# Performance work log

Hardware: AMD Instinct MI355X
Metric: run time of the kernel (lower is better)

The kernel has to match this reference:

```python
import jax, jax.numpy as jnp
import numpy as np

B, T, D, H, L, F, V = 2, 512, 512, 8, 6, 2048, 32000
EPS = 1e-6


def _ln(x, g, b):
    m = x.mean(-1, keepdims=True)
    v = ((x - m) ** 2).mean(-1, keepdims=True)
    return (x - m) / jnp.sqrt(v + EPS) * g + b


def _mha(qx, kx, qkv_w, qkv_b, ow, ob, mask):
    # Wide heads: each head has dim D (Linear(D, H*D) projections, Linear(H*D, D) output).
    Bq, Tq, _ = qx.shape
    def proj(xx, w, bi):
        return (xx @ w + bi).reshape(Bq, Tq, H, D).transpose(0, 2, 1, 3)  # (B,H,T,D)
    q = proj(qx, qkv_w[0], qkv_b[0])
    k = proj(kx, qkv_w[1], qkv_b[1])
    v = proj(kx, qkv_w[2], qkv_b[2])
    s = jnp.einsum('bhqd,bhkd->bhqk', q, k) / jnp.sqrt(jnp.float32(D))
    if mask is not None:
        s = jnp.where(mask, s, -jnp.inf)
    w = jax.nn.softmax(s, axis=-1)
    o = jnp.einsum('bhqk,bhkd->bhqd', w, v).transpose(0, 2, 1, 3).reshape(Bq, Tq, H * D)
    return o @ ow + ob


def _pe(t, d):
    pos = jnp.arange(t, dtype=jnp.float32)[:, None]
    wl = jnp.exp(jnp.arange(0, d, 2, dtype=jnp.float32) / d * -jnp.log(10000.0))
    pe = jnp.zeros((t, d), dtype=jnp.float32)
    pe = pe.at[:, 0::2].set(jnp.sin(pos * wl))
    pe = pe.at[:, 1::2].set(jnp.cos(pos * wl))
    return pe


def _forward(x, y, enc_emb, dec_emb, enc_qkv_w, enc_qkv_b, enc_out_w, enc_out_b,
             enc_ln1_g, enc_ln1_b, enc_ff_w1, enc_ff_b1, enc_ff_w2, enc_ff_b2,
             enc_ln2_g, enc_ln2_b, dec_sa_qkv_w, dec_sa_qkv_b, dec_sa_out_w, dec_sa_out_b,
             dec_ln1_g, dec_ln1_b, dec_ca_qkv_w, dec_ca_qkv_b, dec_ca_out_w, dec_ca_out_b,
             dec_ln2_g, dec_ln2_b, dec_ff_w1, dec_ff_b1, dec_ff_w2, dec_ff_b2,
             dec_ln3_g, dec_ln3_b, head_w, head_b):
    pe = _pe(T, D)
    scale = jnp.sqrt(jnp.float32(D))
    # ---- encoder ----
    h = enc_emb[x] * scale + pe  # (B,T,D)
    for i in range(L):
        a = _mha(h, h, enc_qkv_w[i], enc_qkv_b[i], enc_out_w[i], enc_out_b[i], None)
        h = _ln(a + h, enc_ln1_g[i], enc_ln1_b[i])
        f = jax.nn.relu(h @ enc_ff_w1[i] + enc_ff_b1[i]) @ enc_ff_w2[i] + enc_ff_b2[i]
        h = _ln(f + h, enc_ln2_g[i], enc_ln2_b[i])
    # ---- decoder ----
    causal = jnp.tril(jnp.ones((T, T), dtype=bool))[None, None]  # (1,1,T,T)
    d = dec_emb[y] * scale + pe
    for i in range(L):
        a = _mha(d, d, dec_sa_qkv_w[i], dec_sa_qkv_b[i], dec_sa_out_w[i], dec_sa_out_b[i], causal)
        d = _ln(a + d, dec_ln1_g[i], dec_ln1_b[i])
        c = _mha(d, h, dec_ca_qkv_w[i], dec_ca_qkv_b[i], dec_ca_out_w[i], dec_ca_out_b[i], None)
        d = _ln(c + d, dec_ln2_g[i], dec_ln2_b[i])
        f = jax.nn.relu(d @ dec_ff_w1[i] + dec_ff_b1[i]) @ dec_ff_w2[i] + dec_ff_b2[i]
        d = _ln(f + d, dec_ln3_g[i], dec_ln3_b[i])
    return d @ head_w + head_b  # (B,T,V) logits


def setup_inputs() -> dict:
    key = jax.random.key(0)
    ks = iter(jax.random.split(key, 40))
    def nrm(shape):
        return jax.random.normal(next(ks), shape, dtype=jnp.float32) * 0.02
    HD = H * D
    return {
        'x': jax.random.randint(next(ks), (B, T), 0, V, dtype=jnp.int32),
        'y': jax.random.randint(next(ks), (B, T), 0, V, dtype=jnp.int32),
        'enc_emb': nrm((V, D)), 'dec_emb': nrm((V, D)),
        'enc_qkv_w': nrm((L, 3, D, HD)), 'enc_qkv_b': jnp.zeros((L, 3, HD)),
        'enc_out_w': nrm((L, HD, D)), 'enc_out_b': jnp.zeros((L, D)),
        'enc_ln1_g': jnp.ones((L, D)), 'enc_ln1_b': jnp.zeros((L, D)),
        'enc_ff_w1': nrm((L, D, F)), 'enc_ff_b1': jnp.zeros((L, F)),
        'enc_ff_w2': nrm((L, F, D)), 'enc_ff_b2': jnp.zeros((L, D)),
        'enc_ln2_g': jnp.ones((L, D)), 'enc_ln2_b': jnp.zeros((L, D)),
        'dec_sa_qkv_w': nrm((L, 3, D, HD)), 'dec_sa_qkv_b': jnp.zeros((L, 3, HD)),
        'dec_sa_out_w': nrm((L, HD, D)), 'dec_sa_out_b': jnp.zeros((L, D)),
        'dec_ln1_g': jnp.ones((L, D)), 'dec_ln1_b': jnp.zeros((L, D)),
        'dec_ca_qkv_w': nrm((L, 3, D, HD)), 'dec_ca_qkv_b': jnp.zeros((L, 3, HD)),
        'dec_ca_out_w': nrm((L, HD, D)), 'dec_ca_out_b': jnp.zeros((L, D)),
        'dec_ln2_g': jnp.ones((L, D)), 'dec_ln2_b': jnp.zeros((L, D)),
        'dec_ff_w1': nrm((L, D, F)), 'dec_ff_b1': jnp.zeros((L, F)),
        'dec_ff_w2': nrm((L, F, D)), 'dec_ff_b2': jnp.zeros((L, D)),
        'dec_ln3_g': jnp.ones((L, D)), 'dec_ln3_b': jnp.zeros((L, D)),
        'head_w': nrm((D, V)), 'head_b': jnp.zeros((V,)),
    }


def reference(x, y, enc_emb, dec_emb, enc_qkv_w, enc_qkv_b, enc_out_w, enc_out_b,
              enc_ln1_g, enc_ln1_b, enc_ff_w1, enc_ff_b1, enc_ff_w2, enc_ff_b2,
              enc_ln2_g, enc_ln2_b, dec_sa_qkv_w, dec_sa_qkv_b, dec_sa_out_w, dec_sa_out_b,
              dec_ln1_g, dec_ln1_b, dec_ca_qkv_w, dec_ca_qkv_b, dec_ca_out_w, dec_ca_out_b,
              dec_ln2_g, dec_ln2_b, dec_ff_w1, dec_ff_b1, dec_ff_w2, dec_ff_b2,
              dec_ln3_g, dec_ln3_b, head_w, head_b):
    return _forward(x, y, enc_emb, dec_emb, enc_qkv_w, enc_qkv_b, enc_out_w, enc_out_b,
                    enc_ln1_g, enc_ln1_b, enc_ff_w1, enc_ff_b1, enc_ff_w2, enc_ff_b2,
                    enc_ln2_g, enc_ln2_b, dec_sa_qkv_w, dec_sa_qkv_b, dec_sa_out_w, dec_sa_out_b,
                    dec_ln1_g, dec_ln1_b, dec_ca_qkv_w, dec_ca_qkv_b, dec_ca_out_w, dec_ca_out_b,
                    dec_ln2_g, dec_ln2_b, dec_ff_w1, dec_ff_b1, dec_ff_w2, dec_ff_b2,
                    dec_ln3_g, dec_ln3_b, head_w, head_b)
```

## Files before the change

kernel.cpp:

```cpp
#include <hip/hip_runtime.h>
#include <hip/hip_bf16.h>

#define B_ 2
#define T_ 512
#define D_ 512
#define H_ 8
#define L_ 6
#define F_ 2048
#define V_ 32000
#define BT_ (B_ * T_)
#define HD_ (H_ * D_)
#define BH_ (B_ * H_)

typedef __attribute__((ext_vector_type(8))) short short8;
typedef __attribute__((ext_vector_type(4))) short short4v;
typedef __attribute__((ext_vector_type(4))) float f32x4;

__device__ __forceinline__ short f2b(float f) {
  __hip_bfloat16 h = __float2bfloat16(f);
  short u; __builtin_memcpy(&u, &h, 2); return u;
}
__device__ __forceinline__ void store_c(float* p, float v) { *p = v; }
__device__ __forceinline__ void store_c(short* p, float v) { *p = f2b(v); }

__global__ __launch_bounds__(256) void embed_kernel(
    const int* __restrict__ tok, const float* __restrict__ emb,
    float* __restrict__ out, short* __restrict__ out16)
{
  const int row = blockIdx.x;
  const int t = row & (T_ - 1);
  const int token = tok[row];
  const float* e = emb + (size_t)token * D_;
  float* o = out + (size_t)row * D_;
  short* o16 = out16 + (size_t)row * D_;
  const float scale = sqrtf((float)D_);
  const float nl = -logf(10000.0f);
  for (int d = threadIdx.x; d < D_; d += 256) {
    int i = d >> 1;
    float wl = expf(nl * (2.0f * (float)i) / (float)D_);
    float ang = (float)t * wl;
    float pe = (d & 1) ? cosf(ang) : sinf(ang);
    float v = e[d] * scale + pe;
    o[d] = v; o16[d] = f2b(v);
  }
}

template<bool BTM, typename OutT, int BM>
__global__ __launch_bounds__(256, 3) void mfma_gemm(
    const short* __restrict__ A, long lda, long a_hi, long a_lo,
    const void* __restrict__ Bv, long ldb, long b_hi, long b_lo,
    OutT* __restrict__ C, long ldc, long c_hi, long c_lo, long pstride,
    short* __restrict__ Ct, int trans_hh,
    int K, int nh, int ksplit, float scale,
    const float* __restrict__ bias, long bias_stride)
{
  constexpr int SA = BM + 1;
  constexpr int AU = BM / 32;
  constexpr int WRN = (BM == 128) ? 2 : 1;
  constexpr int WN  = 128 / (4 / WRN);
  constexpr int NR  = WN / 16;
  __shared__ short8 As8[8 * SA];
  __shared__ short8 Bs8[8 * 129];
  const int tid = threadIdx.x;
  const int bh = blockIdx.z / ksplit;
  const int kz = blockIdx.z - bh * ksplit;
  const int bb = bh / nh, hh = bh - bb * nh;
  const short* Ab = A + (long)bb * a_hi + (long)hh * a_lo;
  const short* Bbs = (const short*)Bv + (long)bb * b_hi + (long)hh * b_lo;
  const float* Bbf = (const float*)Bv + (long)bb * b_hi + (long)hh * b_lo;
  OutT* Cb = C + (long)bb * c_hi + (long)hh * c_lo + (long)kz * pstride;

  const int gx = gridDim.x, gy = gridDim.y;
  const int nwg = gx * gy;
  int lin = blockIdx.y * gx + blockIdx.x;
  {
    const int xcd = lin & 7, idx = lin >> 3;
    const int q = nwg >> 3, r = nwg & 7;
    lin = (xcd < r ? xcd * (q + 1) : r * (q + 1) + (xcd - r) * q) + idx;
  }
  const int bn = (lin / gy) * 128;
  const int bm = (lin % gy) * BM;

  const int klen = K / ksplit, kbase = kz * klen;
  const int lane = tid & 63, wid = tid >> 6;
  const int wr = (WRN == 2) ? (wid >> 1) : 0;
  const int wc = (WRN == 2) ? (wid & 1) : wid;
  const int lg = lane >> 4, r16 = lane & 15;

  int arow[AU], acol[AU];
#pragma unroll
  for (int u = 0; u < AU; ++u) { int o = u * 256 + tid; arow[u] = o >> 3; acol[u] = o & 7; }
  const int ncol = tid & 127, nsh = tid >> 7;

  short8 pa[AU];
  short8 pbt[4];
  float  pbn[4][8];

  auto load = [&](int k0) {
#pragma unroll
    for (int u = 0; u < AU; ++u)
      pa[u] = *(const short8*)(Ab + (long)(bm + arow[u]) * lda + (k0 + acol[u] * 8));
    if constexpr (BTM) {
#pragma unroll
      for (int u = 0; u < 4; ++u)
        pbt[u] = *(const short8*)(Bbs + (long)(bn + (u * 256 + tid) / 8) * ldb + (k0 + ((u * 256 + tid) & 7) * 8));
    } else {
      const float* s = Bbf + (long)(k0 + nsh * 32) * ldb + (bn + ncol);
#pragma unroll
      for (int i = 0; i < 4; ++i)
#pragma unroll
        for (int j = 0; j < 8; ++j)
          pbn[i][j] = s[(long)(i * 8 + j) * ldb];
    }
  };
  auto stage = [&]() {
#pragma unroll
    for (int u = 0; u < AU; ++u) As8[acol[u] * SA + arow[u]] = pa[u];
    if constexpr (BTM) {
#pragma unroll
      for (int u = 0; u < 4; ++u)
        Bs8[((u * 256 + tid) & 7) * 129 + (u * 256 + tid) / 8] = pbt[u];
    } else {
#pragma unroll
      for (int i = 0; i < 4; ++i) {
        short8 v;
#pragma unroll
        for (int j = 0; j < 8; ++j) v[j] = f2b(pbn[i][j]);
        Bs8[(nsh * 4 + i) * 129 + ncol] = v;
      }
    }
  };

  f32x4 acc[4][NR] = {};
  auto domfma = [&]() {
#pragma unroll
    for (int kb = 0; kb < 2; ++kb) {
      const int cha = (kb * 4 + lg) * SA;
      const int chb = (kb * 4 + lg) * 129;
      short8 a0 = As8[cha + wr * 64 +  0 + r16];
      short8 a1 = As8[cha + wr * 64 + 16 + r16];
      short8 a2 = As8[cha + wr * 64 + 32 + r16];
      short8 a3 = As8[cha + wr * 64 + 48 + r16];
#pragma unroll
      for (int n = 0; n < NR; ++n) {
        short8 bfr = Bs8[chb + wc * WN + n * 16 + r16];
        acc[0][n] = __builtin_amdgcn_mfma_f32_16x16x32_bf16(a0, bfr, acc[0][n], 0, 0, 0);
        acc[1][n] = __builtin_amdgcn_mfma_f32_16x16x32_bf16(a1, bfr, acc[1][n], 0, 0, 0);
        acc[2][n] = __builtin_amdgcn_mfma_f32_16x16x32_bf16(a2, bfr, acc[2][n], 0, 0, 0);
        acc[3][n] = __builtin_amdgcn_mfma_f32_16x16x32_bf16(a3, bfr, acc[3][n], 0, 0, 0);
      }
    }
  };

  load(kbase);
  stage();
  __syncthreads();
  const int nsteps = klen >> 6;
  for (int t = 0; t < nsteps; ++t) {
    const bool more = (t + 1 < nsteps);
    if (more) load(kbase + (t + 1) * 64);
    domfma();
    if (more) { __syncthreads(); stage(); __syncthreads(); }
  }

  const float* bp = bias ? bias + (long)hh * bias_stride : nullptr;
  if (hh == trans_hh) {
#pragma unroll
    for (int m = 0; m < 4; ++m)
#pragma unroll
      for (int n = 0; n < NR; ++n) {
        const int col = bn + wc * WN + n * 16 + r16;
        const float badd = bp ? bp[col] : 0.0f;
        short4v sv;
#pragma unroll
        for (int rr = 0; rr < 4; ++rr) sv[rr] = f2b(acc[m][n][rr] * scale + badd);
        *(short4v*)(Ct + (long)col * BT_ + (bm + wr * 64 + m * 16 + lg * 4)) = sv;
      }
  } else {
#pragma unroll
    for (int m = 0; m < 4; ++m)
#pragma unroll
      for (int rr = 0; rr < 4; ++rr) {
        const int row = bm + wr * 64 + m * 16 + lg * 4 + rr;
        OutT* crow = Cb + (long)row * ldc + bn + wc * WN + r16;
#pragma unroll
        for (int n = 0; n < NR; ++n) {
          float v = acc[m][n][rr] * scale;
          if (bp) v += bp[bn + wc * WN + n * 16 + r16];
          store_c(&crow[n * 16], v);
        }
      }
  }
}

__global__ __launch_bounds__(256) void reduce_bias_relu_bf16(
    const float* __restrict__ P, long pstride, int ks,
    const float* __restrict__ bias, short* __restrict__ out, long mn, int N)
{
  const long i = ((long)blockIdx.x * 256 + threadIdx.x) * 4;
  if (i >= mn) return;
  float4 s = *(const float4*)(P + i);
  for (int z = 1; z < ks; ++z) {
    float4 t = *(const float4*)(P + (long)z * pstride + i);
    s.x += t.x; s.y += t.y; s.z += t.z; s.w += t.w;
  }
  const int col = (int)(i % N);
  s.x += bias[col]; s.y += bias[col + 1]; s.z += bias[col + 2]; s.w += bias[col + 3];
  short4v o;
  o[0] = f2b(fmaxf(s.x, 0.f)); o[1] = f2b(fmaxf(s.y, 0.f));
  o[2] = f2b(fmaxf(s.z, 0.f)); o[3] = f2b(fmaxf(s.w, 0.f));
  *(short4v*)(out + i) = o;
}

__global__ __launch_bounds__(256) void reduce_ln_kernel(
    const float* __restrict__ P, long pstride, int ks,
    const float* __restrict__ bias, float* __restrict__ hbuf, short* __restrict__ h16,
    const float* __restrict__ gam, const float* __restrict__ bet)
{
  __shared__ float red[256];
  const int row = blockIdx.x, tid = threadIdx.x;
  const long base = (long)row * D_;
  float s0 = hbuf[base + tid] + bias[tid];
  float s1 = hbuf[base + tid + 256] + bias[tid + 256];
  for (int z = 0; z < ks; ++z) {
    s0 += P[(long)z * pstride + base + tid];
    s1 += P[(long)z * pstride + base + tid + 256];
  }
  red[tid] = s0 + s1; __syncthreads();
  for (int o = 128; o > 0; o >>= 1) { if (tid < o) red[tid] += red[tid + o]; __syncthreads(); }
  const float mean = red[0] * (1.0f / D_); __syncthreads();
  const float d0 = s0 - mean, d1 = s1 - mean;
  red[tid] = d0 * d0 + d1 * d1; __syncthreads();
  for (int o = 128; o > 0; o >>= 1) { if (tid < o) red[tid] += red[tid + o]; __syncthreads(); }
  const float inv = rsqrtf(red[0] * (1.0f / D_) + 1e-6f);
  const float v0 = d0 * inv * gam[tid] + bet[tid];
  const float v1 = d1 * inv * gam[tid + 256] + bet[tid + 256];
  hbuf[base + tid] = v0;       h16[base + tid] = f2b(v0);
  hbuf[base + tid + 256] = v1; h16[base + tid + 256] = f2b(v1);
}

__global__ __launch_bounds__(256) void softmax_kernel(
    const float* __restrict__ S, short* __restrict__ P, int causal)
{
  __shared__ float red[256];
  const int q = blockIdx.x, bh = blockIdx.y, tid = threadIdx.x;
  const float* row = S + ((size_t)bh * T_ + q) * T_;
  short* prow = P + ((size_t)bh * T_ + q) * T_;
  const int n = causal ? (q + 1) : T_;
  const float v0 = row[tid], v1 = row[tid + 256];
  const bool in0 = tid < n, in1 = (tid + 256) < n;
  red[tid] = fmaxf(in0 ? v0 : -3.0e38f, in1 ? v1 : -3.0e38f);
  __syncthreads();
  for (int o = 128; o > 0; o >>= 1) { if (tid < o) red[tid] = fmaxf(red[tid], red[tid + o]); __syncthreads(); }
  const float m = red[0]; __syncthreads();
  const float e0 = in0 ? expf(v0 - m) : 0.0f;
  const float e1 = in1 ? expf(v1 - m) : 0.0f;
  red[tid] = e0 + e1; __syncthreads();
  for (int o = 128; o > 0; o >>= 1) { if (tid < o) red[tid] += red[tid + o]; __syncthreads(); }
  const float inv = 1.0f / red[0];
  prow[tid] = f2b(e0 * inv);
  prow[tid + 256] = f2b(e1 * inv);
}

extern "C" void kernel_launch(void* const* d_in, const int* in_sizes, int n_in,
                              void* d_out, int out_size, void* d_ws, size_t ws_size,
                              hipStream_t stream)
{
  const int*   x         = (const int*)d_in[0];
  const int*   y         = (const int*)d_in[1];
  const float* enc_emb   = (const float*)d_in[2];
  const float* dec_emb   = (const float*)d_in[3];
  const float* enc_qkv_w = (const float*)d_in[4];
  const float* enc_qkv_b = (const float*)d_in[5];
  const float* enc_out_w = (const float*)d_in[6];
  const float* enc_out_b = (const float*)d_in[7];
  const float* enc_ln1_g = (const float*)d_in[8];
  const float* enc_ln1_b = (const float*)d_in[9];
  const float* enc_ff_w1 = (const float*)d_in[10];
  const float* enc_ff_b1 = (const float*)d_in[11];
  const float* enc_ff_w2 = (const float*)d_in[12];
  const float* enc_ff_b2 = (const float*)d_in[13];
  const float* enc_ln2_g = (const float*)d_in[14];
  const float* enc_ln2_b = (const float*)d_in[15];
  const float* dec_sa_qkv_w = (const float*)d_in[16];
  const float* dec_sa_qkv_b = (const float*)d_in[17];
  const float* dec_sa_out_w = (const float*)d_in[18];
  const float* dec_sa_out_b = (const float*)d_in[19];
  const float* dec_ln1_g = (const float*)d_in[20];
  const float* dec_ln1_b = (const float*)d_in[21];
  const float* dec_ca_qkv_w = (const float*)d_in[22];
  const float* dec_ca_qkv_b = (const float*)d_in[23];
  const float* dec_ca_out_w = (const float*)d_in[24];
  const float* dec_ca_out_b = (const float*)d_in[25];
  const float* dec_ln2_g = (const float*)d_in[26];
  const float* dec_ln2_b = (const float*)d_in[27];
  const float* dec_ff_w1 = (const float*)d_in[28];
  const float* dec_ff_b1 = (const float*)d_in[29];
  const float* dec_ff_w2 = (const float*)d_in[30];
  const float* dec_ff_b2 = (const float*)d_in[31];
  const float* dec_ln3_g = (const float*)d_in[32];
  const float* dec_ln3_b = (const float*)d_in[33];
  const float* head_w    = (const float*)d_in[34];
  const float* head_b    = (const float*)d_in[35];
  float* out = (float*)d_out;

  char* wsb = (char*)d_ws;
  size_t off = 0;
  auto carve = [&](size_t bytes) { char* p = wsb + off; off += (bytes + 255) & ~255ull; return p; };
  float* h    = (float*)carve((size_t)BT_ * D_ * 4);
  float* dd   = (float*)carve((size_t)BT_ * D_ * 4);
  short* hb16 = (short*)carve((size_t)BT_ * D_ * 2);
  short* db16 = (short*)carve((size_t)BT_ * D_ * 2);
  short* Qb   = (short*)carve((size_t)BT_ * HD_ * 2);
  short* Kb   = (short*)carve((size_t)BT_ * HD_ * 2);
  short* Vt   = (short*)carve((size_t)HD_ * BT_ * 2);
  float* Sb   = (float*)carve((size_t)BH_ * T_ * T_ * 4);
  short* Pb   = (short*)carve((size_t)BH_ * T_ * T_ * 2);
  short* Ob   = Qb;
  short* mid  = Qb;
  (void)ws_size;

  dim3 blk(256);
  const long TT  = (long)T_ * T_;
  const long THD = (long)T_ * HD_;
  const long WQKV = (long)D_ * HD_;

  auto gemm = [&](bool bt, bool of32, bool bm64,
                  const short* A, long lda, long a_hi, long a_lo,
                  const void* Bp, long ldb, long b_hi, long b_lo,
                  void* Cp, long ldc, long c_hi, long c_lo, long pstride,
                  short* Ct, int trans_hh,
                  int M, int N, int K, int batch, int nh, int ksplit,
                  float scale, const float* bias, long bstride) {
    dim3 grd(N / 128, M / (bm64 ? 64 : 128), batch * ksplit);
    if (bm64) {
      if (bt) {
        if (of32) mfma_gemm<true , float, 64><<<grd, blk, 0, stream>>>(A, lda, a_hi, a_lo, Bp, ldb, b_hi, b_lo,
            (float*)Cp, ldc, c_hi, c_lo, pstride, Ct, trans_hh, K, nh, ksplit, scale, bias, bstride);
        else      mfma_gemm<true , short, 64><<<grd, blk, 0, stream>>>(A, lda, a_hi, a_lo, Bp, ldb, b_hi, b_lo,
            (short*)Cp, ldc, c_hi, c_lo, pstride, Ct, trans_hh, K, nh, ksplit, scale, bias, bstride);
      } else {
        if (of32) mfma_gemm<false, float, 64><<<grd, blk, 0, stream>>>(A, lda, a_hi, a_lo, Bp, ldb, b_hi, b_lo,
            (float*)Cp, ldc, c_hi, c_lo, pstride, Ct, trans_hh, K, nh, ksplit, scale, bias, bstride);
        else      mfma_gemm<false, short, 64><<<grd, blk, 0, stream>>>(A, lda, a_hi, a_lo, Bp, ldb, b_hi, b_lo,
            (short*)Cp, ldc, c_hi, c_lo, pstride, Ct, trans_hh, K, nh, ksplit, scale, bias, bstride);
      }
    } else {
      if (of32) mfma_gemm<false, float, 128><<<grd, blk, 0, stream>>>(A, lda, a_hi, a_lo, Bp, ldb, b_hi, b_lo,
          (float*)Cp, ldc, c_hi, c_lo, pstride, Ct, trans_hh, K, nh, ksplit, scale, bias, bstride);
      else      mfma_gemm<false, short, 128><<<grd, blk, 0, stream>>>(A, lda, a_hi, a_lo, Bp, ldb, b_hi, b_lo,
          (short*)Cp, ldc, c_hi, c_lo, pstride, Ct, trans_hh, K, nh, ksplit, scale, bias, bstride);
    }
  };

  auto attention = [&](const short* qsrc, const short* kvsrc, bool self,
                       const float* qkvw, const float* qkvb,
                       const float* ow, const float* ob,
                       float* resid, short* resid16, int causal,
                       const float* lng, const float* lnb) {
    if (self) {
      gemm(false, false, true, qsrc, D_, 0, 0, qkvw, HD_, 0, WQKV,
           Qb, HD_, 0, (long)(Kb - Qb), 0, Vt, 2,
           BT_, HD_, D_, 3, 3, 1, 1.0f, qkvb, HD_);
    } else {
      gemm(false, false, true, qsrc, D_, 0, 0, qkvw, HD_, 0, 0,
           Qb, HD_, 0, 0, 0, nullptr, -1,
           BT_, HD_, D_, 1, 1, 1, 1.0f, qkvb, 0);
      gemm(false, false, true, kvsrc, D_, 0, 0, qkvw + WQKV, HD_, 0, WQKV,
           Kb, HD_, 0, 0, 0, Vt, 1,
           BT_, HD_, D_, 2, 2, 1, 1.0f, qkvb + HD_, HD_);
    }
    gemm(true, true, true, Qb, HD_, THD, D_, Kb, HD_, THD, D_,
         Sb, T_, (long)H_ * TT, TT, 0, nullptr, -1,
         T_, T_, D_, BH_, H_, 1, 0.044194173824159216f, nullptr, 0);
    softmax_kernel<<<dim3(T_, BH_), blk, 0, stream>>>(Sb, Pb, causal);
    gemm(true, false, true, Pb, T_, (long)H_ * TT, TT, Vt, BT_, T_, (long)D_ * BT_,
         Ob, HD_, THD, D_, 0, nullptr, -1,
         T_, D_, T_, BH_, H_, 1, 1.0f, nullptr, 0);
    gemm(false, true, true, Ob, HD_, 0, 0, ow, D_, 0, 0,
         Sb, D_, 0, 0, (long)BT_ * D_, nullptr, -1,
         BT_, D_, HD_, 1, 1, 8, 1.0f, nullptr, 0);
    reduce_ln_kernel<<<dim3(BT_), blk, 0, stream>>>(
        Sb, (long)BT_ * D_, 8, ob, resid, resid16, lng, lnb);
  };

  auto ffn = [&](float* resid, short* resid16,
                 const float* w1, const float* b1,
                 const float* w2, const float* b2,
                 const float* lng, const float* lnb) {
    gemm(false, true, true, resid16, D_, 0, 0, w1, F_, 0, 0,
         Sb, F_, 0, 0, (long)BT_ * F_, nullptr, -1,
         BT_, F_, D_, 1, 1, 2, 1.0f, nullptr, 0);
    reduce_bias_relu_bf16<<<dim3(BT_ * F_ / 1024), blk, 0, stream>>>(
        Sb, (long)BT_ * F_, 2, b1, mid, (long)BT_ * F_, F_);
    gemm(false, true, true, mid, F_, 0, 0, w2, D_, 0, 0,
         Sb, D_, 0, 0, (long)BT_ * D_, nullptr, -1,
         BT_, D_, F_, 1, 1, 8, 1.0f, nullptr, 0);
    reduce_ln_kernel<<<dim3(BT_), blk, 0, stream>>>(
        Sb, (long)BT_ * D_, 8, b2, resid, resid16, lng, lnb);
  };

  embed_kernel<<<dim3(BT_), blk, 0, stream>>>(x, enc_emb, h, hb16);
  for (int i = 0; i < L_; ++i) {
    attention(hb16, hb16, true,
              enc_qkv_w + (size_t)i * 3 * WQKV, enc_qkv_b + (size_t)i * 3 * HD_,
              enc_out_w + (size_t)i * HD_ * D_, enc_out_b + (size_t)i * D_,
              h, hb16, 0, enc_ln1_g + (size_t)i * D_, enc_ln1_b + (size_t)i * D_);
    ffn(h, hb16, enc_ff_w1 + (size_t)i * D_ * F_, enc_ff_b1 + (size_t)i * F_,
        enc_ff_w2 + (size_t)i * F_ * D_, enc_ff_b2 + (size_t)i * D_,
        enc_ln2_g + (size_t)i * D_, enc_ln2_b + (size_t)i * D_);
  }

  embed_kernel<<<dim3(BT_), blk, 0, stream>>>(y, dec_emb, dd, db16);
  for (int i = 0; i < L_; ++i) {
    attention(db16, db16, true,
              dec_sa_qkv_w + (size_t)i * 3 * WQKV, dec_sa_qkv_b + (size_t)i * 3 * HD_,
              dec_sa_out_w + (size_t)i * HD_ * D_, dec_sa_out_b + (size_t)i * D_,
              dd, db16, 1, dec_ln1_g + (size_t)i * D_, dec_ln1_b + (size_t)i * D_);
    attention(db16, hb16, false,
              dec_ca_qkv_w + (size_t)i * 3 * WQKV, dec_ca_qkv_b + (size_t)i * 3 * HD_,
              dec_ca_out_w + (size_t)i * HD_ * D_, dec_ca_out_b + (size_t)i * D_,
              dd, db16, 0, dec_ln2_g + (size_t)i * D_, dec_ln2_b + (size_t)i * D_);
    ffn(dd, db16, dec_ff_w1 + (size_t)i * D_ * F_, dec_ff_b1 + (size_t)i * F_,
        dec_ff_w2 + (size_t)i * F_ * D_, dec_ff_b2 + (size_t)i * D_,
        dec_ln3_g + (size_t)i * D_, dec_ln3_b + (size_t)i * D_);
  }

  gemm(false, true, false, db16, D_, 0, 0, head_w, V_, 0, 0,
       out, V_, 0, 0, 0, nullptr, -1,
       BT_, V_, D_, 1, 1, 1, 1.0f, head_b, 0);
}
```

Baseline: 2.392 ms.

## Double-buffer GEMM LDS tiles, fuse FFN bias+ReLU, switch most GEMMs to 128-row tiles

The GEMM kernel now keeps two LDS buffers and two register prefetch sets, so global loads for the next two K-steps overlap the MFMA work and one barrier is saved per step. FFN1 drops its split-K fp32 partials and the separate bias/ReLU reduce kernel, writing bf16 output with bias and ReLU applied in the epilogue. Most attention and projection GEMMs move from 64-row to 128-row tiles, which adds transposed-B 128 variants and lowers launch bounds to 2 waves for those tiles. The cost is doubled LDS and more registers, which cuts occupancy and leaves fewer blocks for the smaller GEMMs.

New measurement: 2.465 ms. 3.0% more time.

```diff
diff --git a/kernel.cpp b/kernel.cpp
--- a/kernel.cpp
+++ b/kernel.cpp
@@ -46,21 +46,21 @@
 }
 
 template<bool BTM, typename OutT, int BM>
-__global__ __launch_bounds__(256, 3) void mfma_gemm(
+__global__ __launch_bounds__(256, BM == 128 ? 2 : 3) void mfma_gemm(
     const short* __restrict__ A, long lda, long a_hi, long a_lo,
     const void* __restrict__ Bv, long ldb, long b_hi, long b_lo,
     OutT* __restrict__ C, long ldc, long c_hi, long c_lo, long pstride,
-    short* __restrict__ Ct, int trans_hh,
+    short* __restrict__ Ct, int trans_hh, int relu,
     int K, int nh, int ksplit, float scale,
     const float* __restrict__ bias, long bias_stride)
 {
   constexpr int SA = BM + 1;
   constexpr int AU = BM / 32;
   constexpr int WRN = (BM == 128) ? 2 : 1;
-  constexpr int WN  = 128 / (4 / WRN);
+  constexpr int WN  = (BM == 128) ? 64 : 32;
   constexpr int NR  = WN / 16;
-  __shared__ short8 As8[8 * SA];
-  __shared__ short8 Bs8[8 * 129];
+  __shared__ short8 As8[2 * 8 * SA];
+  __shared__ short8 Bs8[2 * 8 * 129];
   const int tid = threadIdx.x;
   const int bh = blockIdx.z / ksplit;
   const int kz = blockIdx.z - bh * ksplit;
@@ -90,53 +90,60 @@
   int arow[AU], acol[AU];
 #pragma unroll
   for (int u = 0; u < AU; ++u) { int o = u * 256 + tid; arow[u] = o >> 3; acol[u] = o & 7; }
+  int brow[4], bcol[4];
+#pragma unroll
+  for (int u = 0; u < 4; ++u) { int o = u * 256 + tid; brow[u] = o >> 3; bcol[u] = o & 7; }
   const int ncol = tid & 127, nsh = tid >> 7;
 
-  short8 pa[AU];
-  short8 pbt[4];
-  float  pbn[4][8];
-
-  auto load = [&](int k0) {
-#pragma unroll
-    for (int u = 0; u < AU; ++u)
-      pa[u] = *(const short8*)(Ab + (long)(bm + arow[u]) * lda + (k0 + acol[u] * 8));
-    if constexpr (BTM) {
-#pragma unroll
-      for (int u = 0; u < 4; ++u)
-        pbt[u] = *(const short8*)(Bbs + (long)(bn + (u * 256 + tid) / 8) * ldb + (k0 + ((u * 256 + tid) & 7) * 8));
-    } else {
-      const float* s = Bbf + (long)(k0 + nsh * 32) * ldb + (bn + ncol);
-#pragma unroll
-      for (int i = 0; i < 4; ++i)
-#pragma unroll
-        for (int j = 0; j < 8; ++j)
-          pbn[i][j] = s[(long)(i * 8 + j) * ldb];
-    }
-  };
-  auto stage = [&]() {
-#pragma unroll
-    for (int u = 0; u < AU; ++u) As8[acol[u] * SA + arow[u]] = pa[u];
-    if constexpr (BTM) {
-#pragma unroll
-      for (int u = 0; u < 4; ++u)
-        Bs8[((u * 256 + tid) & 7) * 129 + (u * 256 + tid) / 8] = pbt[u];
-    } else {
-#pragma unroll
-      for (int i = 0; i < 4; ++i) {
-        short8 v;
-#pragma unroll
-        for (int j = 0; j < 8; ++j) v[j] = f2b(pbn[i][j]);
-        Bs8[(nsh * 4 + i) * 129 + ncol] = v;
-      }
-    }
-  };
+  short8 pa0[AU], pa1[AU];
+  short8 pbt0[4], pbt1[4];
+  float  pbn0[4][8], pbn1[4][8];
+
+#define LOADSET(PA, PBT, PBN, K0)                                               \
+  {                                                                             \
+    _Pragma("unroll")                                                           \
+    for (int u = 0; u < AU; ++u)                                                \
+      PA[u] = *(const short8*)(Ab + (long)(bm + arow[u]) * lda + ((K0) + acol[u] * 8)); \
+    if constexpr (BTM) {                                                        \
+      _Pragma("unroll")                                                         \
+      for (int u = 0; u < 4; ++u)                                               \
+        PBT[u] = *(const short8*)(Bbs + (long)(bn + brow[u]) * ldb + ((K0) + bcol[u] * 8)); \
+    } else {                                                                    \
+      const float* s_ = Bbf + (long)((K0) + nsh * 32) * ldb + (bn + ncol);      \
+      _Pragma("unroll")                                                         \
+      for (int i = 0; i < 4; ++i)                                               \
+        _Pragma("unroll")                                                       \
+        for (int j = 0; j < 8; ++j)                                             \
+          PBN[i][j] = s_[(long)(i * 8 + j) * ldb];                              \
+    }                                                                           \
+  }
+
+#define STAGESET(PA, PBT, PBN, BUF)                                             \
+  {                                                                             \
+    const int ao_ = (BUF) * 8 * SA, bo_ = (BUF) * 8 * 129;                      \
+    _Pragma("unroll")                                                           \
+    for (int u = 0; u < AU; ++u) As8[ao_ + acol[u] * SA + arow[u]] = PA[u];     \
+    if constexpr (BTM) {                                                        \
+      _Pragma("unroll")                                                         \
+      for (int u = 0; u < 4; ++u) Bs8[bo_ + bcol[u] * 129 + brow[u]] = PBT[u];  \
+    } else {                                                                    \
+      _Pragma("unroll")                                                         \
+      for (int i = 0; i < 4; ++i) {                                             \
+        short8 v_;                                                              \
+        _Pragma("unroll")                                                       \
+        for (int j = 0; j < 8; ++j) v_[j] = f2b(PBN[i][j]);                     \
+        Bs8[bo_ + (nsh * 4 + i) * 129 + ncol] = v_;                             \
+      }                                                                         \
+    }                                                                           \
+  }
 
   f32x4 acc[4][NR] = {};
-  auto domfma = [&]() {
+  auto domfma = [&](int buf) {
+    const int ao = buf * 8 * SA, bo = buf * 8 * 129;
 #pragma unroll
     for (int kb = 0; kb < 2; ++kb) {
-      const int cha = (kb * 4 + lg) * SA;
-      const int chb = (kb * 4 + lg) * 129;
+      const int cha = ao + (kb * 4 + lg) * SA;
+      const int chb = bo + (kb * 4 + lg) * 129;
       short8 a0 = As8[cha + wr * 64 +  0 + r16];
       short8 a1 = As8[cha + wr * 64 + 16 + r16];
       short8 a2 = As8[cha + wr * 64 + 32 + r16];
@@ -152,16 +159,26 @@
     }
   };
 
-  load(kbase);
-  stage();
+  const int nsteps = klen >> 6;
+  LOADSET(pa0, pbt0, pbn0, kbase)
+  STAGESET(pa0, pbt0, pbn0, 0)
+  if (nsteps > 1) LOADSET(pa1, pbt1, pbn1, kbase + 64)
   __syncthreads();
-  const int nsteps = klen >> 6;
-  for (int t = 0; t < nsteps; ++t) {
-    const bool more = (t + 1 < nsteps);
-    if (more) load(kbase + (t + 1) * 64);
-    domfma();
-    if (more) { __syncthreads(); stage(); __syncthreads(); }
-  }
+
+  for (int t = 0; t + 1 < nsteps; t += 2) {
+    if (t + 2 < nsteps) LOADSET(pa0, pbt0, pbn0, kbase + (t + 2) * 64)
+    domfma(0);
+    STAGESET(pa1, pbt1, pbn1, 1)
+    __syncthreads();
+    if (t + 3 < nsteps) LOADSET(pa1, pbt1, pbn1, kbase + (t + 3) * 64)
+    domfma(1);
+    if (t + 2 < nsteps) {
+      STAGESET(pa0, pbt0, pbn0, 0)
+      __syncthreads();
+    }
+  }
+#undef LOADSET
+#undef STAGESET
 
   const float* bp = bias ? bias + (long)hh * bias_stride : nullptr;
   if (hh == trans_hh) {
@@ -187,29 +204,11 @@
         for (int n = 0; n < NR; ++n) {
           float v = acc[m][n][rr] * scale;
           if (bp) v += bp[bn + wc * WN + n * 16 + r16];
+          if (relu) v = fmaxf(v, 0.0f);
           store_c(&crow[n * 16], v);
         }
       }
   }
-}
-
-__global__ __launch_bounds__(256) void reduce_bias_relu_bf16(
-    const float* __restrict__ P, long pstride, int ks,
-    const float* __restrict__ bias, short* __restrict__ out, long mn, int N)
-{
-  const long i = ((long)blockIdx.x * 256 + threadIdx.x) * 4;
-  if (i >= mn) return;
-  float4 s = *(const float4*)(P + i);
-  for (int z = 1; z < ks; ++z) {
-    float4 t = *(const float4*)(P + (long)z * pstride + i);
-    s.x += t.x; s.y += t.y; s.z += t.z; s.w += t.w;
-  }
-  const int col = (int)(i % N);
-  s.x += bias[col]; s.y += bias[col + 1]; s.z += bias[col + 2]; s.w += bias[col + 3];
-  short4v o;
-  o[0] = f2b(fmaxf(s.x, 0.f)); o[1] = f2b(fmaxf(s.y, 0.f));
-  o[2] = f2b(fmaxf(s.z, 0.f)); o[3] = f2b(fmaxf(s.w, 0.f));
-  *(short4v*)(out + i) = o;
 }
 
 __global__ __launch_bounds__(256) void reduce_ln_kernel(
@@ -325,7 +324,7 @@
   const long THD = (long)T_ * HD_;
   const long WQKV = (long)D_ * HD_;
 
-  auto gemm = [&](bool bt, bool of32, bool bm64,
+  auto gemm = [&](bool bt, bool of32, bool bm64, int relu,
                   const short* A, long lda, long a_hi, long a_lo,
                   const void* Bp, long ldb, long b_hi, long b_lo,
                   void* Cp, long ldc, long c_hi, long c_lo, long pstride,
@@ -336,20 +335,27 @@
     if (bm64) {
       if (bt) {
         if (of32) mfma_gemm<true , float, 64><<<grd, blk, 0, stream>>>(A, lda, a_hi, a_lo, Bp, ldb, b_hi, b_lo,
-            (float*)Cp, ldc, c_hi, c_lo, pstride, Ct, trans_hh, K, nh, ksplit, scale, bias, bstride);
+            (float*)Cp, ldc, c_hi, c_lo, pstride, Ct, trans_hh, relu, K, nh, ksplit, scale, bias, bstride);
         else      mfma_gemm<true , short, 64><<<grd, blk, 0, stream>>>(A, lda, a_hi, a_lo, Bp, ldb, b_hi, b_lo,
-            (short*)Cp, ldc, c_hi, c_lo, pstride, Ct, trans_hh, K, nh, ksplit, scale, bias, bstride);
+            (short*)Cp, ldc, c_hi, c_lo, pstride, Ct, trans_hh, relu, K, nh, ksplit, scale, bias, bstride);
       } else {
         if (of32) mfma_gemm<false, float, 64><<<grd, blk, 0, stream>>>(A, lda, a_hi, a_lo, Bp, ldb, b_hi, b_lo,
-            (float*)Cp, ldc, c_hi, c_lo, pstride, Ct, trans_hh, K, nh, ksplit, scale, bias, bstride);
+            (float*)Cp, ldc, c_hi, c_lo, pstride, Ct, trans_hh, relu, K, nh, ksplit, scale, bias, bstride);
         else      mfma_gemm<false, short, 64><<<grd, blk, 0, stream>>>(A, lda, a_hi, a_lo, Bp, ldb, b_hi, b_lo,
-            (short*)Cp, ldc, c_hi, c_lo, pstride, Ct, trans_hh, K, nh, ksplit, scale, bias, bstride);
+            (short*)Cp, ldc, c_hi, c_lo, pstride, Ct, trans_hh, relu, K, nh, ksplit, scale, bias, bstride);
       }
     } else {
-      if (of32) mfma_gemm<false, float, 128><<<grd, blk, 0, stream>>>(A, lda, a_hi, a_lo, Bp, ldb, b_hi, b_lo,
-          (float*)Cp, ldc, c_hi, c_lo, pstride, Ct, trans_hh, K, nh, ksplit, scale, bias, bstride);
-      else      mfma_gemm<false, short, 128><<<grd, blk, 0, stream>>>(A, lda, a_hi, a_lo, Bp, ldb, b_hi, b_lo,
-          (short*)Cp, ldc, c_hi, c_lo, pstride, Ct, trans_hh, K, nh, ksplit, scale, bias, bstride);
+      if (bt) {
+        if (of32) mfma_gemm<true , float, 128><<<grd, blk, 0, stream>>>(A, lda, a_hi, a_lo, Bp, ldb, b_hi, b_lo,
+            (float*)Cp, ldc, c_hi, c_lo, pstride, Ct, trans_hh, relu, K, nh, ksplit, scale, bias, bstride);
+        else      mfma_gemm<true , short, 128><<<grd, blk, 0, stream>>>(A, lda, a_hi, a_lo, Bp, ldb, b_hi, b_lo,
+            (short*)Cp, ldc, c_hi, c_lo, pstride, Ct, trans_hh, relu, K, nh, ksplit, scale, bias, bstride);
+      } else {
+        if (of32) mfma_gemm<false, float, 128><<<grd, blk, 0, stream>>>(A, lda, a_hi, a_lo, Bp, ldb, b_hi, b_lo,
+            (float*)Cp, ldc, c_hi, c_lo, pstride, Ct, trans_hh, relu, K, nh, ksplit, scale, bias, bstride);
+        else      mfma_gemm<false, short, 128><<<grd, blk, 0, stream>>>(A, lda, a_hi, a_lo, Bp, ldb, b_hi, b_lo,
+            (short*)Cp, ldc, c_hi, c_lo, pstride, Ct, trans_hh, relu, K, nh, ksplit, scale, bias, bstride);
+      }
     }
   };
 
@@ -359,25 +365,25 @@
                        float* resid, short* resid16, int causal,
                        const float* lng, const float* lnb) {
     if (self) {
-      gemm(false, false, true, qsrc, D_, 0, 0, qkvw, HD_, 0, WQKV,
+      gemm(false, false, false, 0, qsrc, D_, 0, 0, qkvw, HD_, 0, WQKV,
            Qb, HD_, 0, (long)(Kb - Qb), 0, Vt, 2,
            BT_, HD_, D_, 3, 3, 1, 1.0f, qkvb, HD_);
     } else {
-      gemm(false, false, true, qsrc, D_, 0, 0, qkvw, HD_, 0, 0,
+      gemm(false, false, false, 0, qsrc, D_, 0, 0, qkvw, HD_, 0, 0,
            Qb, HD_, 0, 0, 0, nullptr, -1,
            BT_, HD_, D_, 1, 1, 1, 1.0f, qkvb, 0);
-      gemm(false, false, true, kvsrc, D_, 0, 0, qkvw + WQKV, HD_, 0, WQKV,
+      gemm(false, false, false, 0, kvsrc, D_, 0, 0, qkvw + WQKV, HD_, 0, WQKV,
            Kb, HD_, 0, 0, 0, Vt, 1,
            BT_, HD_, D_, 2, 2, 1, 1.0f, qkvb + HD_, HD_);
     }
-    gemm(true, true, true, Qb, HD_, THD, D_, Kb, HD_, THD, D_,
+    gemm(true, true, false, 0, Qb, HD_, THD, D_, Kb, HD_, THD, D_,
          Sb, T_, (long)H_ * TT, TT, 0, nullptr, -1,
          T_, T_, D_, BH_, H_, 1, 0.044194173824159216f, nullptr, 0);
     softmax_kernel<<<dim3(T_, BH_), blk, 0, stream>>>(Sb, Pb, causal);
-    gemm(true, false, true, Pb, T_, (long)H_ * TT, TT, Vt, BT_, T_, (long)D_ * BT_,
+    gemm(true, false, false, 0, Pb, T_, (long)H_ * TT, TT, Vt, BT_, T_, (long)D_ * BT_,
          Ob, HD_, THD, D_, 0, nullptr, -1,
          T_, D_, T_, BH_, H_, 1, 1.0f, nullptr, 0);
-    gemm(false, true, true, Ob, HD_, 0, 0, ow, D_, 0, 0,
+    gemm(false, true, false, 0, Ob, HD_, 0, 0, ow, D_, 0, 0,
          Sb, D_, 0, 0, (long)BT_ * D_, nullptr, -1,
          BT_, D_, HD_, 1, 1, 8, 1.0f, nullptr, 0);
     reduce_ln_kernel<<<dim3(BT_), blk, 0, stream>>>(
@@ -388,12 +394,10 @@
                  const float* w1, const float* b1,
                  const float* w2, const float* b2,
                  const float* lng, const float* lnb) {
-    gemm(false, true, true, resid16, D_, 0, 0, w1, F_, 0, 0,
-         Sb, F_, 0, 0, (long)BT_ * F_, nullptr, -1,
-         BT_, F_, D_, 1, 1, 2, 1.0f, nullptr, 0);
-    reduce_bias_relu_bf16<<<dim3(BT_ * F_ / 1024), blk, 0, stream>>>(
-        Sb, (long)BT_ * F_, 2, b1, mid, (long)BT_ * F_, F_);
-    gemm(false, true, true, mid, F_, 0, 0, w2, D_, 0, 0,
+    gemm(false, false, true, 1, resid16, D_, 0, 0, w1, F_, 0, 0,
+         mid, F_, 0, 0, 0, nullptr, -1,
+         BT_, F_, D_, 1, 1, 1, 1.0f, b1, 0);
+    gemm(false, true, false, 0, mid, F_, 0, 0, w2, D_, 0, 0,
          Sb, D_, 0, 0, (long)BT_ * D_, nullptr, -1,
          BT_, D_, F_, 1, 1, 8, 1.0f, nullptr, 0);
     reduce_ln_kernel<<<dim3(BT_), blk, 0, stream>>>(
@@ -426,7 +430,7 @@
         dec_ln3_g + (size_t)i * D_, dec_ln3_b + (size_t)i * D_);
   }
 
-  gemm(false, true, false, db16, D_, 0, 0, head_w, V_, 0, 0,
+  gemm(false, true, false, 0, db16, D_, 0, 0, head_w, V_, 0, 0,
        out, V_, 0, 0, 0, nullptr, -1,
        BT_, V_, D_, 1, 1, 1, 1.0f, head_b, 0);
 }
```

## Fuse QK^T with softmax in one kernel and fuse FFN bias+ReLU into GEMM

Applied to the files above, without the earlier changes.

Adds a qksm_kernel that computes Q·K^T scores with MFMA, then applies scaling, causal masking and softmax in registers and writes bf16 probabilities. This replaces the fp32 score GEMM and the separate softmax kernel, and causal blocks skip key tiles that are fully masked. The first FFN GEMM now adds bias and applies ReLU in its epilogue and writes bf16 directly, instead of split-K fp32 partials followed by a reduce kernel. The fused attention kernel holds 32 accumulator tiles per wave and reloads K into LDS for each of 8 chunks, which may raise register pressure and lower occupancy.

Measured after the change: 3.162 ms. +32.2%, slower.

```diff
diff --git a/kernel.cpp b/kernel.cpp
--- a/kernel.cpp
+++ b/kernel.cpp
@@ -50,14 +50,14 @@
     const short* __restrict__ A, long lda, long a_hi, long a_lo,
     const void* __restrict__ Bv, long ldb, long b_hi, long b_lo,
     OutT* __restrict__ C, long ldc, long c_hi, long c_lo, long pstride,
-    short* __restrict__ Ct, int trans_hh,
+    short* __restrict__ Ct, int trans_hh, int relu,
     int K, int nh, int ksplit, float scale,
     const float* __restrict__ bias, long bias_stride)
 {
   constexpr int SA = BM + 1;
   constexpr int AU = BM / 32;
   constexpr int WRN = (BM == 128) ? 2 : 1;
-  constexpr int WN  = 128 / (4 / WRN);
+  constexpr int WN  = (BM == 128) ? 64 : 32;
   constexpr int NR  = WN / 16;
   __shared__ short8 As8[8 * SA];
   __shared__ short8 Bs8[8 * 129];
@@ -90,6 +90,9 @@
   int arow[AU], acol[AU];
 #pragma unroll
   for (int u = 0; u < AU; ++u) { int o = u * 256 + tid; arow[u] = o >> 3; acol[u] = o & 7; }
+  int brow[4], bcol[4];
+#pragma unroll
+  for (int u = 0; u < 4; ++u) { int o = u * 256 + tid; brow[u] = o >> 3; bcol[u] = o & 7; }
   const int ncol = tid & 127, nsh = tid >> 7;
 
   short8 pa[AU];
@@ -103,7 +106,7 @@
     if constexpr (BTM) {
 #pragma unroll
       for (int u = 0; u < 4; ++u)
-        pbt[u] = *(const short8*)(Bbs + (long)(bn + (u * 256 + tid) / 8) * ldb + (k0 + ((u * 256 + tid) & 7) * 8));
+        pbt[u] = *(const short8*)(Bbs + (long)(bn + brow[u]) * ldb + (k0 + bcol[u] * 8));
     } else {
       const float* s = Bbf + (long)(k0 + nsh * 32) * ldb + (bn + ncol);
 #pragma unroll
@@ -118,8 +121,7 @@
     for (int u = 0; u < AU; ++u) As8[acol[u] * SA + arow[u]] = pa[u];
     if constexpr (BTM) {
 #pragma unroll
-      for (int u = 0; u < 4; ++u)
-        Bs8[((u * 256 + tid) & 7) * 129 + (u * 256 + tid) / 8] = pbt[u];
+      for (int u = 0; u < 4; ++u) Bs8[bcol[u] * 129 + brow[u]] = pbt[u];
     } else {
 #pragma unroll
       for (int i = 0; i < 4; ++i) {
@@ -187,29 +189,133 @@
         for (int n = 0; n < NR; ++n) {
           float v = acc[m][n][rr] * scale;
           if (bp) v += bp[bn + wc * WN + n * 16 + r16];
+          if (relu) v = fmaxf(v, 0.0f);
           store_c(&crow[n * 16], v);
         }
       }
   }
 }
 
-__global__ __launch_bounds__(256) void reduce_bias_relu_bf16(
-    const float* __restrict__ P, long pstride, int ks,
-    const float* __restrict__ bias, short* __restrict__ out, long mn, int N)
+__global__ __launch_bounds__(256, 2) void qksm_kernel(
+    const short* __restrict__ Q, const short* __restrict__ Kg,
+    short* __restrict__ P, int causal)
 {
-  const long i = ((long)blockIdx.x * 256 + threadIdx.x) * 4;
-  if (i >= mn) return;
-  float4 s = *(const float4*)(P + i);
-  for (int z = 1; z < ks; ++z) {
-    float4 t = *(const float4*)(P + (long)z * pstride + i);
-    s.x += t.x; s.y += t.y; s.z += t.z; s.w += t.w;
-  }
-  const int col = (int)(i % N);
-  s.x += bias[col]; s.y += bias[col + 1]; s.z += bias[col + 2]; s.w += bias[col + 3];
-  short4v o;
-  o[0] = f2b(fmaxf(s.x, 0.f)); o[1] = f2b(fmaxf(s.y, 0.f));
-  o[2] = f2b(fmaxf(s.z, 0.f)); o[3] = f2b(fmaxf(s.w, 0.f));
-  *(short4v*)(out + i) = o;
+  __shared__ short8 Buf[4224];
+  short* LDSP = (short*)Buf;
+
+  const int tid = threadIdx.x;
+  const int lane = tid & 63, w = tid >> 6;
+  const int lg = lane >> 4, r16 = lane & 15;
+
+  int lin = blockIdx.y * 8 + blockIdx.x;
+  { const int xcd = lin & 7, idx = lin >> 3; lin = xcd * 16 + idx; }
+  const int bh = lin >> 3, qt = lin & 7;
+  const int b = bh >> 3, hh = bh & 7;
+  const int q0 = qt * 64;
+
+  const int nlim = causal ? (qt * 4 + w + 1) : 32;
+  const int ntok = causal ? (q0 + 64) : T_;
+
+  const short* Qrow = Q + ((long)b * T_ + q0 + w * 16 + r16) * HD_ + hh * D_;
+  short8 qf[8][2];
+#pragma unroll
+  for (int s = 0; s < 8; ++s)
+#pragma unroll
+    for (int kb = 0; kb < 2; ++kb)
+      qf[s][kb] = *(const short8*)(Qrow + s * 64 + kb * 32 + lg * 8);
+
+  const short* Kbase = Kg + ((long)b * T_) * HD_ + hh * D_;
+
+  f32x4 sacc[32];
+#pragma unroll
+  for (int n = 0; n < 32; ++n) sacc[n] = (f32x4){0.f, 0.f, 0.f, 0.f};
+
+#pragma unroll
+  for (int s = 0; s < 8; ++s) {
+#pragma unroll
+    for (int i = 0; i < 16; ++i) {
+      int idx = i * 256 + tid;
+      int tok = idx >> 3, c = idx & 7;
+      if (tok < ntok)
+        Buf[c * 513 + tok] = *(const short8*)(Kbase + (long)tok * HD_ + s * 64 + c * 8);
+    }
+    __syncthreads();
+#pragma unroll
+    for (int kb = 0; kb < 2; ++kb) {
+#pragma unroll
+      for (int n = 0; n < 32; ++n) {
+        if (n < nlim) {
+          short8 bfr = Buf[(kb * 4 + lg) * 513 + n * 16 + r16];
+          sacc[n] = __builtin_amdgcn_mfma_f32_16x16x32_bf16(qf[s][kb], bfr, sacc[n], 0, 0, 0);
+        }
+      }
+    }
+    __syncthreads();
+  }
+
+  const float sscale = 0.044194173824159216f;
+  const int qrow = q0 + w * 16 + lg * 4;
+  float mx[4] = {-3.0e38f, -3.0e38f, -3.0e38f, -3.0e38f};
+#pragma unroll
+  for (int n = 0; n < 32; ++n) {
+    if (n < nlim) {
+      const int col = n * 16 + r16;
+#pragma unroll
+      for (int rr = 0; rr < 4; ++rr) {
+        float v = sacc[n][rr] * sscale;
+        if (causal && col > qrow + rr) v = -3.0e38f;
+        sacc[n][rr] = v;
+        mx[rr] = fmaxf(mx[rr], v);
+      }
+    }
+  }
+#pragma unroll
+  for (int rr = 0; rr < 4; ++rr) {
+    mx[rr] = fmaxf(mx[rr], __shfl_xor(mx[rr], 1));
+    mx[rr] = fmaxf(mx[rr], __shfl_xor(mx[rr], 2));
+    mx[rr] = fmaxf(mx[rr], __shfl_xor(mx[rr], 4));
+    mx[rr] = fmaxf(mx[rr], __shfl_xor(mx[rr], 8));
+  }
+  float sum[4] = {0.f, 0.f, 0.f, 0.f};
+#pragma unroll
+  for (int n = 0; n < 32; ++n) {
+    if (n < nlim) {
+#pragma unroll
+      for (int rr = 0; rr < 4; ++rr) {
+        float p = expf(sacc[n][rr] - mx[rr]);
+        sacc[n][rr] = p;
+        sum[rr] += p;
+      }
+    }
+  }
+#pragma unroll
+  for (int rr = 0; rr < 4; ++rr) {
+    sum[rr] += __shfl_xor(sum[rr], 1);
+    sum[rr] += __shfl_xor(sum[rr], 2);
+    sum[rr] += __shfl_xor(sum[rr], 4);
+    sum[rr] += __shfl_xor(sum[rr], 8);
+  }
+  float inv[4];
+#pragma unroll
+  for (int rr = 0; rr < 4; ++rr) inv[rr] = 1.0f / sum[rr];
+
+#pragma unroll
+  for (int n = 0; n < 32; ++n) {
+    const int col = n * 16 + r16;
+#pragma unroll
+    for (int rr = 0; rr < 4; ++rr) {
+      float val = (n < nlim) ? sacc[n][rr] * inv[rr] : 0.0f;
+      LDSP[(w * 16 + lg * 4 + rr) * 528 + col] = f2b(val);
+    }
+  }
+  __syncthreads();
+  short* Pout = P + (long)bh * T_ * T_ + (long)q0 * T_;
+#pragma unroll
+  for (int i = 0; i < 16; ++i) {
+    int idx = i * 256 + tid;
+    int row = idx >> 6, c8 = idx & 63;
+    *(short8*)(Pout + (long)row * T_ + c8 * 8) = *(short8*)(LDSP + row * 528 + c8 * 8);
+  }
 }
 
 __global__ __launch_bounds__(256) void reduce_ln_kernel(
@@ -237,29 +343,6 @@
   const float v1 = d1 * inv * gam[tid + 256] + bet[tid + 256];
   hbuf[base + tid] = v0;       h16[base + tid] = f2b(v0);
   hbuf[base + tid + 256] = v1; h16[base + tid + 256] = f2b(v1);
-}
-
-__global__ __launch_bounds__(256) void softmax_kernel(
-    const float* __restrict__ S, short* __restrict__ P, int causal)
-{
-  __shared__ float red[256];
-  const int q = blockIdx.x, bh = blockIdx.y, tid = threadIdx.x;
-  const float* row = S + ((size_t)bh * T_ + q) * T_;
-  short* prow = P + ((size_t)bh * T_ + q) * T_;
-  const int n = causal ? (q + 1) : T_;
-  const float v0 = row[tid], v1 = row[tid + 256];
-  const bool in0 = tid < n, in1 = (tid + 256) < n;
-  red[tid] = fmaxf(in0 ? v0 : -3.0e38f, in1 ? v1 : -3.0e38f);
-  __syncthreads();
-  for (int o = 128; o > 0; o >>= 1) { if (tid < o) red[tid] = fmaxf(red[tid], red[tid + o]); __syncthreads(); }
-  const float m = red[0]; __syncthreads();
-  const float e0 = in0 ? expf(v0 - m) : 0.0f;
-  const float e1 = in1 ? expf(v1 - m) : 0.0f;
-  red[tid] = e0 + e1; __syncthreads();
-  for (int o = 128; o > 0; o >>= 1) { if (tid < o) red[tid] += red[tid + o]; __syncthreads(); }
-  const float inv = 1.0f / red[0];
-  prow[tid] = f2b(e0 * inv);
-  prow[tid + 256] = f2b(e1 * inv);
 }
 
 extern "C" void kernel_launch(void* const* d_in, const int* in_sizes, int n_in,
@@ -321,11 +404,10 @@
   (void)ws_size;
 
   dim3 blk(256);
-  const long TT  = (long)T_ * T_;
   const long THD = (long)T_ * HD_;
   const long WQKV = (long)D_ * HD_;
 
-  auto gemm = [&](bool bt, bool of32, bool bm64,
+  auto gemm = [&](bool bt, bool of32, bool bm64, int relu,
                   const short* A, long lda, long a_hi, long a_lo,
                   const void* Bp, long ldb, long b_hi, long b_lo,
                   void* Cp, long ldc, long c_hi, long c_lo, long pstride,
@@ -336,20 +418,27 @@
     if (bm64) {
       if (bt) {
         if (of32) mfma_gemm<true , float, 64><<<grd, blk, 0, stream>>>(A, lda, a_hi, a_lo, Bp, ldb, b_hi, b_lo,
-            (float*)Cp, ldc, c_hi, c_lo, pstride, Ct, trans_hh, K, nh, ksplit, scale, bias, bstride);
+            (float*)Cp, ldc, c_hi, c_lo, pstride, Ct, trans_hh, relu, K, nh, ksplit, scale, bias, bstride);
         else      mfma_gemm<true , short, 64><<<grd, blk, 0, stream>>>(A, lda, a_hi, a_lo, Bp, ldb, b_hi, b_lo,
-            (short*)Cp, ldc, c_hi, c_lo, pstride, Ct, trans_hh, K, nh, ksplit, scale, bias, bstride);
+            (short*)Cp, ldc, c_hi, c_lo, pstride, Ct, trans_hh, relu, K, nh, ksplit, scale, bias, bstride);
       } else {
         if (of32) mfma_gemm<false, float, 64><<<grd, blk, 0, stream>>>(A, lda, a_hi, a_lo, Bp, ldb, b_hi, b_lo,
-            (float*)Cp, ldc, c_hi, c_lo, pstride, Ct, trans_hh, K, nh, ksplit, scale, bias, bstride);
+            (float*)Cp, ldc, c_hi, c_lo, pstride, Ct, trans_hh, relu, K, nh, ksplit, scale, bias, bstride);
         else      mfma_gemm<false, short, 64><<<grd, blk, 0, stream>>>(A, lda, a_hi, a_lo, Bp, ldb, b_hi, b_lo,
-            (short*)Cp, ldc, c_hi, c_lo, pstride, Ct, trans_hh, K, nh, ksplit, scale, bias, bstride);
+            (short*)Cp, ldc, c_hi, c_lo, pstride, Ct, trans_hh, relu, K, nh, ksplit, scale, bias, bstride);
       }
     } else {
-      if (of32) mfma_gemm<false, float, 128><<<grd, blk, 0, stream>>>(A, lda, a_hi, a_lo, Bp, ldb, b_hi, b_lo,
-          (float*)Cp, ldc, c_hi, c_lo, pstride, Ct, trans_hh, K, nh, ksplit, scale, bias, bstride);
-      else      mfma_gemm<false, short, 128><<<grd, blk, 0, stream>>>(A, lda, a_hi, a_lo, Bp, ldb, b_hi, b_lo,
-          (short*)Cp, ldc, c_hi, c_lo, pstride, Ct, trans_hh, K, nh, ksplit, scale, bias, bstride);
+      if (bt) {
+        if (of32) mfma_gemm<true , float, 128><<<grd, blk, 0, stream>>>(A, lda, a_hi, a_lo, Bp, ldb, b_hi, b_lo,
+            (float*)Cp, ldc, c_hi, c_lo, pstride, Ct, trans_hh, relu, K, nh, ksplit, scale, bias, bstride);
+        else      mfma_gemm<true , short, 128><<<grd, blk, 0, stream>>>(A, lda, a_hi, a_lo, Bp, ldb, b_hi, b_lo,
+            (short*)Cp, ldc, c_hi, c_lo, pstride, Ct, trans_hh, relu, K, nh, ksplit, scale, bias, bstride);
+      } else {
+        if (of32) mfma_gemm<false, float, 128><<<grd, blk, 0, stream>>>(A, lda, a_hi, a_lo, Bp, ldb, b_hi, b_lo,
+            (float*)Cp, ldc, c_hi, c_lo, pstride, Ct, trans_hh, relu, K, nh, ksplit, scale, bias, bstride);
+        else      mfma_gemm<false, short, 128><<<grd, blk, 0, stream>>>(A, lda, a_hi, a_lo, Bp, ldb, b_hi, b_lo,
+            (short*)Cp, ldc, c_hi, c_lo, pstride, Ct, trans_hh, relu, K, nh, ksplit, scale, bias, bstride);
+      }
     }
   };
 
@@ -359,25 +448,23 @@
                        float* resid, short* resid16, int causal,
                        const float* lng, const float* lnb) {
     if (self) {
-      gemm(false, false, true, qsrc, D_, 0, 0, qkvw, HD_, 0, WQKV,
+      gemm(false, false, true, 0, qsrc, D_, 0, 0, qkvw, HD_, 0, WQKV,
            Qb, HD_, 0, (long)(Kb - Qb), 0, Vt, 2,
            BT_, HD_, D_, 3, 3, 1, 1.0f, qkvb, HD_);
     } else {
-      gemm(false, false, true, qsrc, D_, 0, 0, qkvw, HD_, 0, 0,
+      gemm(false, false, true, 0, qsrc, D_, 0, 0, qkvw, HD_, 0, 0,
            Qb, HD_, 0, 0, 0, nullptr, -1,
            BT_, HD_, D_, 1, 1, 1, 1.0f, qkvb, 0);
-      gemm(false, false, true, kvsrc, D_, 0, 0, qkvw + WQKV, HD_, 0, WQKV,
+      gemm(false, false, true, 0, kvsrc, D_, 0, 0, qkvw + WQKV, HD_, 0, WQKV,
            Kb, HD_, 0, 0, 0, Vt, 1,
            BT_, HD_, D_, 2, 2, 1, 1.0f, qkvb + HD_, HD_);
     }
-    gemm(true, true, true, Qb, HD_, THD, D_, Kb, HD_, THD, D_,
-         Sb, T_, (long)H_ * TT, TT, 0, nullptr, -1,
-         T_, T_, D_, BH_, H_, 1, 0.044194173824159216f, nullptr, 0);
-    softmax_kernel<<<dim3(T_, BH_), blk, 0, stream>>>(Sb, Pb, causal);
-    gemm(true, false, true, Pb, T_, (long)H_ * TT, TT, Vt, BT_, T_, (long)D_ * BT_,
+    qksm_kernel<<<dim3(T_ / 64, BH_), blk, 0, stream>>>(Qb, Kb, Pb, causal);
+    gemm(true, false, true, 0, Pb, T_, (long)H_ * (long)T_ * T_, (long)T_ * T_,
+         Vt, BT_, T_, (long)D_ * BT_,
          Ob, HD_, THD, D_, 0, nullptr, -1,
          T_, D_, T_, BH_, H_, 1, 1.0f, nullptr, 0);
-    gemm(false, true, true, Ob, HD_, 0, 0, ow, D_, 0, 0,
+    gemm(false, true, true, 0, Ob, HD_, 0, 0, ow, D_, 0, 0,
          Sb, D_, 0, 0, (long)BT_ * D_, nullptr, -1,
          BT_, D_, HD_, 1, 1, 8, 1.0f, nullptr, 0);
     reduce_ln_kernel<<<dim3(BT_), blk, 0, stream>>>(
@@ -388,12 +475,10 @@
                  const float* w1, const float* b1,
                  const float* w2, const float* b2,
                  const float* lng, const float* lnb) {
-    gemm(false, true, true, resid16, D_, 0, 0, w1, F_, 0, 0,
-         Sb, F_, 0, 0, (long)BT_ * F_, nullptr, -1,
-         BT_, F_, D_, 1, 1, 2, 1.0f, nullptr, 0);
-    reduce_bias_relu_bf16<<<dim3(BT_ * F_ / 1024), blk, 0, stream>>>(
-        Sb, (long)BT_ * F_, 2, b1, mid, (long)BT_ * F_, F_);
-    gemm(false, true, true, mid, F_, 0, 0, w2, D_, 0, 0,
+    gemm(false, false, true, 1, resid16, D_, 0, 0, w1, F_, 0, 0,
+         mid, F_, 0, 0, 0, nullptr, -1,
+         BT_, F_, D_, 1, 1, 1, 1.0f, b1, 0);
+    gemm(false, true, true, 0, mid, F_, 0, 0, w2, D_, 0, 0,
          Sb, D_, 0, 0, (long)BT_ * D_, nullptr, -1,
          BT_, D_, F_, 1, 1, 8, 1.0f, nullptr, 0);
     reduce_ln_kernel<<<dim3(BT_), blk, 0, stream>>>(
@@ -426,7 +511,7 @@
         dec_ln3_g + (size_t)i * D_, dec_ln3_b + (size_t)i * D_);
   }
 
-  gemm(false, true, false, db16, D_, 0, 0, head_w, V_, 0, 0,
+  gemm(false, true, false, 0, db16, D_, 0, 0, head_w, V_, 0, 0,
        out, V_, 0, 0, 0, nullptr, -1,
        BT_, V_, D_, 1, 1, 1, 1.0f, head_b, 0);
 }
```
